# Kernel optimization log

Hardware: AMD Instinct MI355X
Metric: run time of the kernel (lower is better)

The kernel has to match this reference:

```python
import jax, jax.numpy as jnp
import numpy as np

K = 20                      # kNN size (init kwarg k)
_BN_S = 1.0 / np.sqrt(1.0 + 1e-5)  # BatchNorm eval with running var=1, mean=0


def _edge_conv(f, W1, b1, g, be, W2, b2):
    # f: [B,N,C]. DynamicEdgeConv: kNN in feature space (self included, as in
    # torch_cluster.knn), message = MLP([x_i, x_j - x_i]), max aggregation.
    sq = jnp.sum(f * f, -1)
    d = sq[:, :, None] + sq[:, None, :] - 2.0 * jnp.einsum('bnc,bmc->bnm', f, f)
    _, idx = jax.lax.top_k(-d, K)                      # [B,N,K]
    fj = jax.vmap(lambda fb, ib: fb[ib])(f, idx)       # [B,N,K,C] neighbor gather
    fi = jnp.broadcast_to(f[:, :, None, :], fj.shape)
    msg = jnp.concatenate([fi, fj - fi], -1)           # [B,N,K,2C]
    h = jax.nn.relu((msg @ W1 + b1) * (g * _BN_S) + be)  # Linear -> BN(eval) -> ReLU
    h = h @ W2 + b2                                    # plain last MLP layer
    return jnp.max(h, axis=2)                          # max over K neighbors


def _forward(x, pos,
             c1_W1, c1_b1, c1_g, c1_be, c1_W2, c1_b2,
             c2_W1, c2_b1, c2_g, c2_be, c2_W2, c2_b2,
             c3_W1, c3_b1, c3_g, c3_be, c3_W2, c3_b2,
             m_W1, m_b1, m_W2, m_b2, m_W3, m_b3, m_W4, m_b4):
    x0 = jnp.concatenate([x, pos], -1)                 # [B,N,6]
    x1 = _edge_conv(x0, c1_W1, c1_b1, c1_g, c1_be, c1_W2, c1_b2)
    x2 = _edge_conv(x1, c2_W1, c2_b1, c2_g, c2_be, c2_W2, c2_b2)
    x3 = _edge_conv(x2, c3_W1, c3_b1, c3_g, c3_be, c3_W2, c3_b2)
    h = jnp.concatenate([x1, x2, x3], -1)              # [B,N,192]
    # head MLP: norm=None, dropout inactive at inference, plain last layer
    h = jax.nn.relu(h @ m_W1 + m_b1)
    h = jax.nn.relu(h @ m_W2 + m_b2)
    h = jax.nn.relu(h @ m_W3 + m_b3)
    out = h @ m_W4 + m_b4                              # [B,N,40]
    return jax.nn.log_softmax(out, -1)


def setup_inputs() -> dict:
    key = jax.random.key(0)
    ks = iter(jax.random.split(key, 40))

    def lin(cin, cout):
        W = jax.random.normal(next(ks), (cin, cout), jnp.float32) / np.sqrt(cin)
        b = jnp.zeros((cout,), jnp.float32)
        return W, b

    inp = {}
    inp['x'] = jax.random.normal(next(ks), (8, 4096, 3), jnp.float32)
    inp['pos'] = jax.random.normal(next(ks), (8, 4096, 3), jnp.float32)
    for i, cin in zip((1, 2, 3), (12, 128, 128)):      # 2*in_channels of each conv
        W1, b1 = lin(cin, 64)
        W2, b2 = lin(64, 64)
        inp[f'c{i}_W1'], inp[f'c{i}_b1'] = W1, b1
        inp[f'c{i}_g'] = jnp.ones((64,), jnp.float32)
        inp[f'c{i}_be'] = jnp.zeros((64,), jnp.float32)
        inp[f'c{i}_W2'], inp[f'c{i}_b2'] = W2, b2
    dims = [192, 1024, 256, 128, 40]
    for j in range(4):
        W, b = lin(dims[j], dims[j + 1])
        inp[f'm_W{j + 1}'], inp[f'm_b{j + 1}'] = W, b
    return inp


def reference(x, pos,
              c1_W1, c1_b1, c1_g, c1_be, c1_W2, c1_b2,
              c2_W1, c2_b1, c2_g, c2_be, c2_W2, c2_b2,
              c3_W1, c3_b1, c3_g, c3_be, c3_W2, c3_b2,
              m_W1, m_b1, m_W2, m_b2, m_W3, m_b3, m_W4, m_b4):
    return _forward(x, pos,
                    c1_W1, c1_b1, c1_g, c1_be, c1_W2, c1_b2,
                    c2_W1, c2_b1, c2_g, c2_be, c2_W2, c2_b2,
                    c3_W1, c3_b1, c3_g, c3_be, c3_W2, c3_b2,
                    m_W1, m_b1, m_W2, m_b2, m_W3, m_b3, m_W4, m_b4)
```

## Files before the change

kernel.cpp:

```cpp
#include <hip/hip_runtime.h>
#include <math.h>

#define KNN 20
#define NPTS 4096
#define NB 8

__device__ __forceinline__ bool lexless(float d1, int i1, float d2, int i2) {
    return d1 < d2 || (d1 == d2 && i1 < i2);
}

__global__ __launch_bounds__(256) void concat_norm_kernel(const float* __restrict__ x,
                                                          const float* __restrict__ pos,
                                                          float* __restrict__ f0,
                                                          float* __restrict__ nrm, int total) {
    int p = blockIdx.x * 256 + threadIdx.x;
    if (p < total) {
        float v0 = x[(size_t)p*3 + 0], v1 = x[(size_t)p*3 + 1], v2 = x[(size_t)p*3 + 2];
        float v3 = pos[(size_t)p*3 + 0], v4 = pos[(size_t)p*3 + 1], v5 = pos[(size_t)p*3 + 2];
        f0[(size_t)p*6 + 0] = v0; f0[(size_t)p*6 + 1] = v1; f0[(size_t)p*6 + 2] = v2;
        f0[(size_t)p*6 + 3] = v3; f0[(size_t)p*6 + 4] = v4; f0[(size_t)p*6 + 5] = v5;
        float s = 0.f;
        s = fmaf(v0, v0, s); s = fmaf(v1, v1, s); s = fmaf(v2, v2, s);
        s = fmaf(v3, v3, s); s = fmaf(v4, v4, s); s = fmaf(v5, v5, s);
        nrm[p] = s;
    }
}

template<int C>
__global__ __launch_bounds__(256) void norm_kernel(const float* __restrict__ f, int ldf,
                                                   float* __restrict__ norms, int total) {
    int p = blockIdx.x * 256 + threadIdx.x;
    if (p >= total) return;
    const float* fp = f + (size_t)p * ldf;
    float s = 0.f;
    if constexpr ((C & 3) == 0) {
#pragma unroll
        for (int k = 0; k < C; k += 4) {
            float4 v = *(const float4*)(fp + k);
            s = fmaf(v.x, v.x, s); s = fmaf(v.y, v.y, s);
            s = fmaf(v.z, v.z, s); s = fmaf(v.w, v.w, s);
        }
    } else {
#pragma unroll
        for (int k = 0; k < C; ++k) s = fmaf(fp[k], fp[k], s);
    }
    norms[p] = s;
}

#define KCHAIN(ck_) do {                                                 \
    unsigned long long kc = (ck_);                                       \
    _Pragma("unroll")                                                    \
    for (int t = 0; t < KNN; ++t) {                                      \
        bool sw = kc < bk[t];                                            \
        unsigned long long nn = sw ? kc : bk[t];                         \
        unsigned long long oo = sw ? bk[t] : kc;                         \
        bk[t] = nn; kc = oo;                                             \
    }                                                                    \
} while (0)

#define PACKK(dv_, jv_, out_) do {                                       \
    unsigned pu = __float_as_uint(dv_);                                  \
    pu = (pu == 0x80000000u) ? 0u : pu;                    \
    pu ^= (unsigned)((int)pu >> 31) | 0x80000000u;                       \
    (out_) = ((unsigned long long)pu << 32) | (unsigned)(jv_);           \
} while (0)

#define PUSHF(dv_, jg_) do {                                             \
    if ((dv_) <= thr) {                                                  \
        pd5 = pd4; pj5 = pj4; pd4 = pd3; pj4 = pj3;                      \
        pd3 = pd2; pj3 = pj2; pd2 = pd1; pj2 = pj1;                      \
        pd1 = pd0; pj1 = pj0; pd0 = (dv_); pj0 = (jg_); ++cnt;           \
    }                                                                    \
} while (0)

#define FLUSHF() do {                                                    \
    if (cnt > 0) { unsigned long long k0_; PACKK(pd0, pj0, k0_); KCHAIN(k0_); } \
    if (cnt > 1) { unsigned long long k1_; PACKK(pd1, pj1, k1_); KCHAIN(k1_); } \
    if (cnt > 2) { unsigned long long k2_; PACKK(pd2, pj2, k2_); KCHAIN(k2_); } \
    if (cnt > 3) { unsigned long long k3_; PACKK(pd3, pj3, k3_); KCHAIN(k3_); } \
    if (cnt > 4) { unsigned long long k4_; PACKK(pd4, pj4, k4_); KCHAIN(k4_); } \
    if (cnt > 5) { unsigned long long k5_; PACKK(pd5, pj5, k5_); KCHAIN(k5_); } \
    cnt = 0;                                                             \
    unsigned hu_ = (unsigned)(bk[KNN - 1] >> 32);                        \
    atomicMin(&thrQ[q], hu_);                                            \
    hu_ = (hu_ & 0x80000000u) ? (hu_ ^ 0x80000000u) : ~hu_;              \
    thr = __uint_as_float(hu_);                                          \
} while (0)

#define KMERGE(ptr_) do {                                                \
    const unsigned long long* mp = (ptr_);                               \
    _Pragma("unroll 1")                                                  \
    for (int tm = 0; tm < KNN; ++tm) {                                   \
        unsigned long long mk = mp[tm];                                  \
        if (mk >= bk[KNN - 1]) break;                                    \
        KCHAIN(mk);                                                      \
    }                                                                    \
} while (0)

#define KSENTINEL 0xFF800000FFFFFFFFULL

template<int C>
__global__ __launch_bounds__(128, 2) void knn_tile_kernel(const float* __restrict__ f, int ldf,
                                                          const float* __restrict__ norms,
                                                          int* __restrict__ idx) {
    const int qb    = blockIdx.x * 32;
    const int b     = qb >> 12;
    const int qloc0 = qb & (NPTS - 1);
    const int tid   = threadIdx.x;
    const int q     = tid & 31;
    const int sub   = tid >> 5;
    const int tx    = tid & 15;
    const int ty    = tid >> 4;

    union __align__(16) SM {
        struct {
            float Qs[C][32];
            float Cs[C][64];
            float Ds[32][68];
        } a;
        unsigned long long md[32][2 * KNN + 1];
    };
    __shared__ SM sm;
    __shared__ unsigned thrQ[32];

    const float* fb = f + (size_t)b * NPTS * ldf;
    const float* nb = norms + (size_t)b * NPTS;

    if (tid < 32) thrQ[tid] = 0xFFFFFFFFu;

    if constexpr ((C & 15) == 0) {
        int m = tid >> 2, ko = (tid & 3) * 4;
        const float* src = fb + (size_t)(qloc0 + m) * ldf;
#pragma unroll
        for (int k4 = ko; k4 < C; k4 += 16) {
            float4 v = *(const float4*)(src + k4);
            sm.a.Qs[k4 + 0][m] = v.x; sm.a.Qs[k4 + 1][m] = v.y;
            sm.a.Qs[k4 + 2][m] = v.z; sm.a.Qs[k4 + 3][m] = v.w;
        }
    } else {
        for (int e = tid; e < C * 32; e += 128) {
            int k = e >> 5, m = e & 31;
            sm.a.Qs[k][m] = fb[(size_t)(qloc0 + m) * ldf + k];
        }
    }

    const float4 qnv = *(const float4*)(nb + qloc0 + ty * 4);
    const float qnr[4] = {qnv.x, qnv.y, qnv.z, qnv.w};

    unsigned long long bk[KNN];
#pragma unroll
    for (int t = 0; t < KNN; ++t) bk[t] = KSENTINEL;
    float thr = INFINITY;
    float pd0 = 0.f, pd1 = 0.f, pd2 = 0.f, pd3 = 0.f, pd4 = 0.f, pd5 = 0.f;
    int   pj0 = 0, pj1 = 0, pj2 = 0, pj3 = 0, pj4 = 0, pj5 = 0;
    int   cnt = 0;

    auto stageC = [&](int j0) {
        if constexpr ((C & 7) == 0) {
            int jj = tid >> 1, ko = (tid & 1) * 4;
            const float* src = fb + (size_t)(j0 + jj) * ldf;
#pragma unroll
            for (int k4 = ko; k4 < C; k4 += 8) {
                float4 v = *(const float4*)(src + k4);
                sm.a.Cs[k4 + 0][jj] = v.x; sm.a.Cs[k4 + 1][jj] = v.y;
                sm.a.Cs[k4 + 2][jj] = v.z; sm.a.Cs[k4 + 3][jj] = v.w;
            }
        } else {
            for (int e = tid; e < C * 64; e += 128) {
                int k = e >> 6, j = e & 63;
                sm.a.Cs[k][j] = fb[(size_t)(j0 + j) * ldf + k];
            }
        }
    };

    auto gemmT = [&](int j0) {
        float acc[4][4] = {};
#pragma unroll 8
        for (int kk = 0; kk < C; ++kk) {
            float4 av = *(const float4*)&sm.a.Qs[kk][ty * 4];
            float4 bv = *(const float4*)&sm.a.Cs[kk][tx * 4];
            float a[4] = {av.x, av.y, av.z, av.w};
            float bb[4] = {bv.x, bv.y, bv.z, bv.w};
#pragma unroll
            for (int i = 0; i < 4; ++i)
#pragma unroll
                for (int j = 0; j < 4; ++j) acc[i][j] = fmaf(a[i], bb[j], acc[i][j]);
        }
        const float4 cnv = *(const float4*)(nb + j0 + tx * 4);
#pragma unroll
        for (int i = 0; i < 4; ++i) {
            float4 o;
            o.x = fmaf(-2.0f, acc[i][0], qnr[i] + cnv.x);
            o.y = fmaf(-2.0f, acc[i][1], qnr[i] + cnv.y);
            o.z = fmaf(-2.0f, acc[i][2], qnr[i] + cnv.z);
            o.w = fmaf(-2.0f, acc[i][3], qnr[i] + cnv.w);
            *(float4*)&sm.a.Ds[ty * 4 + i][tx * 4] = o;
        }
    };

    auto scanT = [&](int j0) {
        {
            unsigned su = thrQ[q];
            unsigned hu = (su & 0x80000000u) ? (su ^ 0x80000000u) : ~su;
            thr = fminf(thr, __uint_as_float(hu));
        }
        const int jb = sub * 16;
        const float4 v0 = *(const float4*)&sm.a.Ds[q][jb + 0];
        const float4 v1 = *(const float4*)&sm.a.Ds[q][jb + 4];
        const float4 v2 = *(const float4*)&sm.a.Ds[q][jb + 8];
        const float4 v3 = *(const float4*)&sm.a.Ds[q][jb + 12];
        const int jg = j0 + jb;
        PUSHF(v0.x, jg + 0);  PUSHF(v0.y, jg + 1);
        PUSHF(v0.z, jg + 2);  PUSHF(v0.w, jg + 3);  if (__any(cnt >= 3)) FLUSHF();
        PUSHF(v1.x, jg + 4);  PUSHF(v1.y, jg + 5);
        PUSHF(v1.z, jg + 6);  PUSHF(v1.w, jg + 7);  if (__any(cnt >= 3)) FLUSHF();
        PUSHF(v2.x, jg + 8);  PUSHF(v2.y, jg + 9);
        PUSHF(v2.z, jg + 10); PUSHF(v2.w, jg + 11); if (__any(cnt >= 3)) FLUSHF();
        PUSHF(v3.x, jg + 12); PUSHF(v3.y, jg + 13);
        PUSHF(v3.z, jg + 14); PUSHF(v3.w, jg + 15);
        if (__any(cnt > 0)) FLUSHF();
    };

    stageC(0);
    __syncthreads();
    gemmT(0);
    __syncthreads();
#pragma unroll 1
    for (int t = 1; t < NPTS / 64; ++t) {
        stageC(t * 64);
        scanT((t - 1) * 64);
        __syncthreads();
        gemmT(t * 64);
        __syncthreads();
    }
    scanT(NPTS - 64);
    if (__any(cnt > 0)) FLUSHF();

    __syncthreads();
    if (sub >= 2) {
#pragma unroll
        for (int t = 0; t < KNN; ++t) sm.md[q][(sub - 2) * KNN + t] = bk[t];
    }
    __syncthreads();
    if (sub < 2) KMERGE(&sm.md[q][sub * KNN]);
    __syncthreads();
    if (sub == 1) {
#pragma unroll
        for (int t = 0; t < KNN; ++t) sm.md[q][t] = bk[t];
    }
    __syncthreads();
    if (sub == 0) {
        KMERGE(&sm.md[q][0]);
        int* op = idx + (size_t)(qb + q) * KNN;
#pragma unroll
        for (int t = 0; t < KNN; ++t) op[t] = (int)bk[t];
    }
}

__global__ __launch_bounds__(128, 2) void knn6_kernel(const float* __restrict__ f,
                                                      const float* __restrict__ norms,
                                                      int* __restrict__ idx) {
    const int qb    = blockIdx.x * 32;
    const int b     = qb >> 12;
    const int qloc0 = qb & (NPTS - 1);
    const int tid   = threadIdx.x;
    const int q     = tid & 31;
    const int sub   = tid >> 5;

    __shared__ __align__(16) float Cs[2][64][8];
    __shared__ unsigned long long md[32][2 * KNN + 1];
    __shared__ unsigned thrQ[32];

    const float* fb = f + (size_t)b * NPTS * 6;
    const float* nb = norms + (size_t)b * NPTS;

    if (tid < 32) thrQ[tid] = 0xFFFFFFFFu;

    float fir[6];
    {
        const float* qsrc = fb + (size_t)(qloc0 + q) * 6;
#pragma unroll
        for (int k = 0; k < 6; ++k) fir[k] = qsrc[k];
    }
    const float qn = nb[qloc0 + q];

    unsigned long long bk[KNN];
#pragma unroll
    for (int t = 0; t < KNN; ++t) bk[t] = KSENTINEL;
    float thr = INFINITY;
    float pd0 = 0.f, pd1 = 0.f, pd2 = 0.f, pd3 = 0.f, pd4 = 0.f, pd5 = 0.f;
    int   pj0 = 0, pj1 = 0, pj2 = 0, pj3 = 0, pj4 = 0, pj5 = 0;
    int   cnt = 0;

    auto stage6 = [&](int j0, int s) {
#pragma unroll
        for (int e = tid; e < 512; e += 128) {
            int j = e >> 3, k = e & 7;
            float v = 0.f;
            if (k < 6)       v = fb[(size_t)(j0 + j) * 6 + k];
            else if (k == 6) v = nb[j0 + j];
            Cs[s][j][k] = v;
        }
    };

    auto scan6 = [&](int j0, int s) {
        {
            unsigned su = thrQ[q];
            unsigned hu = (su & 0x80000000u) ? (su ^ 0x80000000u) : ~su;
            thr = fminf(thr, __uint_as_float(hu));
        }
        const int jb = sub * 16;
#pragma unroll
        for (int jj = 0; jj < 16; ++jj) {
            const float4 c0 = *(const float4*)&Cs[s][jb + jj][0];
            const float4 c1 = *(const float4*)&Cs[s][jb + jj][4];
            float dot = 0.f;
            dot = fmaf(fir[0], c0.x, dot);
            dot = fmaf(fir[1], c0.y, dot);
            dot = fmaf(fir[2], c0.z, dot);
            dot = fmaf(fir[3], c0.w, dot);
            dot = fmaf(fir[4], c1.x, dot);
            dot = fmaf(fir[5], c1.y, dot);
            float d = fmaf(-2.0f, dot, qn + c1.z);
            PUSHF(d, j0 + jb + jj);
            if ((jj & 3) == 3) { if (__any(cnt >= 3)) FLUSHF(); }
        }
        if (__any(cnt > 0)) FLUSHF();
    };

    stage6(0, 0);
    __syncthreads();
#pragma unroll 1
    for (int t = 0; t < NPTS / 64; ++t) {
        const int cur = t & 1;
        if (t + 1 < NPTS / 64) stage6((t + 1) * 64, cur ^ 1);
        scan6(t * 64, cur);
        __syncthreads();
    }
    if (__any(cnt > 0)) FLUSHF();

    if (sub >= 2) {
#pragma unroll
        for (int t = 0; t < KNN; ++t) md[q][(sub - 2) * KNN + t] = bk[t];
    }
    __syncthreads();
    if (sub < 2) KMERGE(&md[q][sub * KNN]);
    __syncthreads();
    if (sub == 1) {
#pragma unroll
        for (int t = 0; t < KNN; ++t) md[q][t] = bk[t];
    }
    __syncthreads();
    if (sub == 0) {
        KMERGE(&md[q][0]);
        int* op = idx + (size_t)(qb + q) * KNN;
#pragma unroll
        for (int t = 0; t < KNN; ++t) op[t] = (int)bk[t];
    }
}

template<int C>
__global__ __launch_bounds__(64) void edgeconv_kernel(
    const float* __restrict__ f, int ldf,
    const int* __restrict__ idx,
    const float* __restrict__ W1, const float* __restrict__ b1,
    const float* __restrict__ g,  const float* __restrict__ be,
    const float* __restrict__ W2, const float* __restrict__ b2,
    float* __restrict__ out, int ldo) {
    const int p = blockIdx.x;
    const int b = p >> 12;
    const int i = p & (NPTS - 1);
    const int c = threadIdx.x;
    __shared__ __align__(16) float fi_s[C];
    __shared__ __align__(16) float fj_s[KNN][C];
    __shared__ __align__(16) float h1_s[KNN][64];
    __shared__ int nidx[KNN];
    const float* fb = f + (size_t)b * NPTS * ldf;
    if (c < KNN) nidx[c] = idx[(size_t)p * KNN + c];
    if (c < C)   fi_s[c] = fb[(size_t)i * ldf + c];
    __syncthreads();
#pragma unroll
    for (int j = 0; j < KNN; ++j)
        if (c < C) fj_s[j][c] = fb[(size_t)nidx[j] * ldf + c];
    __syncthreads();
    float fir[C];
#pragma unroll
    for (int k = 0; k < C; ++k) fir[k] = fi_s[k];

    const float bn_s = (float)(1.0 / sqrt(1.0 + 1e-5));
    const float bnscale = g[c] * bn_s;
    float base = b1[c];
#pragma unroll
    for (int k = 0; k < C; ++k) base = fmaf(fir[k], W1[k * 64 + c], base);
    float acc[KNN];
#pragma unroll
    for (int j = 0; j < KNN; ++j) acc[j] = base;

    if constexpr ((C & 3) == 0) {
#pragma unroll
        for (int k = 0; k < C; k += 4) {
            float w0 = W1[(C + k + 0) * 64 + c];
            float w1 = W1[(C + k + 1) * 64 + c];
            float w2 = W1[(C + k + 2) * 64 + c];
            float w3 = W1[(C + k + 3) * 64 + c];
            float f0 = fir[k + 0], f1 = fir[k + 1], f2 = fir[k + 2], f3 = fir[k + 3];
#pragma unroll
            for (int j = 0; j < KNN; ++j) {
                float4 v = *(const float4*)&fj_s[j][k];
                acc[j] = fmaf(v.x - f0, w0, acc[j]);
                acc[j] = fmaf(v.y - f1, w1, acc[j]);
                acc[j] = fmaf(v.z - f2, w2, acc[j]);
                acc[j] = fmaf(v.w - f3, w3, acc[j]);
            }
        }
    } else {
#pragma unroll
        for (int k = 0; k < C; ++k) {
            float w = W1[(C + k) * 64 + c];
            float fik = fir[k];
#pragma unroll
            for (int j = 0; j < KNN; ++j) acc[j] = fmaf(fj_s[j][k] - fik, w, acc[j]);
        }
    }
    float bec = be[c];
#pragma unroll
    for (int j = 0; j < KNN; ++j) h1_s[j][c] = fmaxf(fmaf(acc[j], bnscale, bec), 0.f);
    __syncthreads();

    float acc2[KNN];
    float b2c = b2[c];
#pragma unroll
    for (int j = 0; j < KNN; ++j) acc2[j] = b2c;
#pragma unroll
    for (int k = 0; k < 64; k += 4) {
        float w0 = W2[(k + 0) * 64 + c];
        float w1 = W2[(k + 1) * 64 + c];
        float w2 = W2[(k + 2) * 64 + c];
        float w3 = W2[(k + 3) * 64 + c];
#pragma unroll
        for (int j = 0; j < KNN; ++j) {
            float4 v = *(const float4*)&h1_s[j][k];
            acc2[j] = fmaf(v.x, w0, acc2[j]);
            acc2[j] = fmaf(v.y, w1, acc2[j]);
            acc2[j] = fmaf(v.z, w2, acc2[j]);
            acc2[j] = fmaf(v.w, w3, acc2[j]);
        }
    }
    float m = acc2[0];
#pragma unroll
    for (int j = 1; j < KNN; ++j) m = fmaxf(m, acc2[j]);
    out[(size_t)p * ldo + c] = m;
}

__global__ __launch_bounds__(256) void repack_w1_kernel(const float* __restrict__ W1,
                                                        const float* __restrict__ b1,
                                                        float* __restrict__ Wp,
                                                        float* __restrict__ bp) {
    int t = blockIdx.x * 256 + threadIdx.x;
    if (t < 64 * 64) {
        int k = t >> 6, c = t & 63;
        Wp[k * 128 + c]      = W1[k * 64 + c];
        Wp[k * 128 + 64 + c] = W1[(64 + k) * 64 + c];
    }
    if (t < 128) bp[t] = (t < 64) ? b1[t] : 0.f;
}

__global__ __launch_bounds__(64) void edgeconv_fact_kernel(
    const float* __restrict__ GH,
    const int* __restrict__ idx,
    const float* __restrict__ g,  const float* __restrict__ be,
    const float* __restrict__ W2, const float* __restrict__ b2,
    float* __restrict__ out, int ldo) {
    const int p = blockIdx.x;
    const int b = p >> 12;
    const int c = threadIdx.x;
    __shared__ __align__(16) float h1_s[KNN][64];
    __shared__ int nidx[KNN];
    if (c < KNN) nidx[c] = idx[(size_t)p * KNN + c];
    const float H = GH[(size_t)p * 128 + c];
    const float G = GH[(size_t)p * 128 + 64 + c];
    const float hb = H - G;
    const float bn_s = (float)(1.0 / sqrt(1.0 + 1e-5));
    const float bnscale = g[c] * bn_s;
    const float bec = be[c];
    const float* GHb = GH + (size_t)b * NPTS * 128 + 64;
    __syncthreads();
#pragma unroll
    for (int j = 0; j < KNN; ++j) {
        float gj = GHb[(size_t)nidx[j] * 128 + c];
        h1_s[j][c] = fmaxf(fmaf(hb + gj, bnscale, bec), 0.f);
    }
    __syncthreads();

    float acc2[KNN];
    float b2c = b2[c];
#pragma unroll
    for (int j = 0; j < KNN; ++j) acc2[j] = b2c;
#pragma unroll
    for (int k = 0; k < 64; k += 4) {
        float w0 = W2[(k + 0) * 64 + c];
        float w1 = W2[(k + 1) * 64 + c];
        float w2 = W2[(k + 2) * 64 + c];
        float w3 = W2[(k + 3) * 64 + c];
#pragma unroll
        for (int j = 0; j < KNN; ++j) {
            float4 v = *(const float4*)&h1_s[j][k];
            acc2[j] = fmaf(v.x, w0, acc2[j]);
            acc2[j] = fmaf(v.y, w1, acc2[j]);
            acc2[j] = fmaf(v.z, w2, acc2[j]);
            acc2[j] = fmaf(v.w, w3, acc2[j]);
        }
    }
    float m = acc2[0];
#pragma unroll
    for (int j = 1; j < KNN; ++j) m = fmaxf(m, acc2[j]);
    out[(size_t)p * ldo + c] = m;
}

template<bool RELU>
__global__ __launch_bounds__(256, 2) void gemm_kernel(
    const float* __restrict__ A, int lda,
    const float* __restrict__ W,
    const float* __restrict__ bias,
    float* __restrict__ Cc, int ldc,
    int N, int K) {
    const int BM = 128, BN = 128, BK = 16;
    __shared__ __align__(16) float As[16][128 + 4];
    __shared__ __align__(16) float Bs[16][128 + 4];
    const int bm = blockIdx.y * BM;
    const int bn = blockIdx.x * BN;
    const int tid = threadIdx.x;
    const int tx = tid & 15, ty = tid >> 4;
    float acc[8][8] = {};
    for (int k0 = 0; k0 < K; k0 += BK) {
        {
            int r = tid >> 2;
            int kq = (tid & 3) * 4;
#pragma unroll
            for (int h = 0; h < 2; ++h) {
                int rr = r + h * 64;
                float4 v = *(const float4*)(A + (size_t)(bm + rr) * lda + k0 + kq);
                As[kq + 0][rr] = v.x; As[kq + 1][rr] = v.y;
                As[kq + 2][rr] = v.z; As[kq + 3][rr] = v.w;
            }
        }
        {
            int kk = tid >> 4;
            int n8 = (tid & 15) * 8;
            float4 v0 = *(const float4*)(W + (size_t)(k0 + kk) * N + bn + n8);
            float4 v1 = *(const float4*)(W + (size_t)(k0 + kk) * N + bn + n8 + 4);
            *(float4*)&Bs[kk][n8] = v0;
            *(float4*)&Bs[kk][n8 + 4] = v1;
        }
        __syncthreads();
#pragma unroll
        for (int kk = 0; kk < BK; ++kk) {
            float4 a0 = *(const float4*)&As[kk][ty * 8];
            float4 a1 = *(const float4*)&As[kk][ty * 8 + 4];
            float4 b0 = *(const float4*)&Bs[kk][tx * 8];
            float4 b1 = *(const float4*)&Bs[kk][tx * 8 + 4];
            float a[8] = {a0.x, a0.y, a0.z, a0.w, a1.x, a1.y, a1.z, a1.w};
            float bb[8] = {b0.x, b0.y, b0.z, b0.w, b1.x, b1.y, b1.z, b1.w};
#pragma unroll
            for (int i = 0; i < 8; ++i)
#pragma unroll
                for (int j = 0; j < 8; ++j) acc[i][j] = fmaf(a[i], bb[j], acc[i][j]);
        }
        __syncthreads();
    }
    const float4 bi0 = *(const float4*)(bias + bn + tx * 8);
    const float4 bi1 = *(const float4*)(bias + bn + tx * 8 + 4);
    const float bb[8] = {bi0.x, bi0.y, bi0.z, bi0.w, bi1.x, bi1.y, bi1.z, bi1.w};
#pragma unroll
    for (int i = 0; i < 8; ++i) {
        int m = bm + ty * 8 + i;
        float4 o0, o1;
        o0.x = acc[i][0] + bb[0]; o0.y = acc[i][1] + bb[1];
        o0.z = acc[i][2] + bb[2]; o0.w = acc[i][3] + bb[3];
        o1.x = acc[i][4] + bb[4]; o1.y = acc[i][5] + bb[5];
        o1.z = acc[i][6] + bb[6]; o1.w = acc[i][7] + bb[7];
        if (RELU) {
            o0.x = fmaxf(o0.x, 0.f); o0.y = fmaxf(o0.y, 0.f);
            o0.z = fmaxf(o0.z, 0.f); o0.w = fmaxf(o0.w, 0.f);
            o1.x = fmaxf(o1.x, 0.f); o1.y = fmaxf(o1.y, 0.f);
            o1.z = fmaxf(o1.z, 0.f); o1.w = fmaxf(o1.w, 0.f);
        }
        *(float4*)(Cc + (size_t)m * ldc + bn + tx * 8) = o0;
        *(float4*)(Cc + (size_t)m * ldc + bn + tx * 8 + 4) = o1;
    }
}

__global__ __launch_bounds__(64) void head_kernel(const float* __restrict__ h3,
                                                  const float* __restrict__ W4,
                                                  const float* __restrict__ b4,
                                                  float* __restrict__ out) {
    const int p = blockIdx.x;
    const int lane = threadIdx.x;
    const float* hp = h3 + (size_t)p * 128;
    float v = -INFINITY;
    if (lane < 40) {
        float acc = b4[lane];
#pragma unroll
        for (int k = 0; k < 128; ++k) acc = fmaf(hp[k], W4[k * 40 + lane], acc);
        v = acc;
    }
    float mx = v;
#pragma unroll
    for (int s = 1; s < 64; s <<= 1) mx = fmaxf(mx, __shfl_xor(mx, s));
    float e = (lane < 40) ? expf(v - mx) : 0.0f;
    float se = e;
#pragma unroll
    for (int s = 1; s < 64; s <<= 1) se += __shfl_xor(se, s);
    if (lane < 40) out[(size_t)p * 40 + lane] = v - mx - logf(se);
}

extern "C" void kernel_launch(void* const* d_in, const int* in_sizes, int n_in,
                              void* d_out, int out_size, void* d_ws, size_t ws_size,
                              hipStream_t stream) {
    (void)in_sizes; (void)n_in; (void)out_size;
    const float* x     = (const float*)d_in[0];
    const float* pos   = (const float*)d_in[1];
    const float* c1_W1 = (const float*)d_in[2];
    const float* c1_b1 = (const float*)d_in[3];
    const float* c1_g  = (const float*)d_in[4];
    const float* c1_be = (const float*)d_in[5];
    const float* c1_W2 = (const float*)d_in[6];
    const float* c1_b2 = (const float*)d_in[7];
    const float* c2_W1 = (const float*)d_in[8];
    const float* c2_b1 = (const float*)d_in[9];
    const float* c2_g  = (const float*)d_in[10];
    const float* c2_be = (const float*)d_in[11];
    const float* c2_W2 = (const float*)d_in[12];
    const float* c2_b2 = (const float*)d_in[13];
    const float* c3_W1 = (const float*)d_in[14];
    const float* c3_b1 = (const float*)d_in[15];
    const float* c3_g  = (const float*)d_in[16];
    const float* c3_be = (const float*)d_in[17];
    const float* c3_W2 = (const float*)d_in[18];
    const float* c3_b2 = (const float*)d_in[19];
    const float* m_W1  = (const float*)d_in[20];
    const float* m_b1  = (const float*)d_in[21];
    const float* m_W2  = (const float*)d_in[22];
    const float* m_b2  = (const float*)d_in[23];
    const float* m_W3  = (const float*)d_in[24];
    const float* m_b3  = (const float*)d_in[25];
    const float* m_W4  = (const float*)d_in[26];
    const float* m_b4  = (const float*)d_in[27];
    float* out = (float*)d_out;

    const int TOT = NB * NPTS;

    float* ws   = (float*)d_ws;
    float* f0   = ws;
    int*   idxb = (int*)(ws + 196608);
    float* feat = ws + 196608 + 655360;

    const size_t basef  = 196608 + 655360 + 6291456;
    const size_t availf = ws_size / 4;
    int MC = 4096;
    if (availf >= basef + (size_t)32768 * 1408) MC = 32768;
    else if (availf >= basef + (size_t)16384 * 1408) MC = 16384;
    else if (availf >= basef + (size_t)8192 * 1408) MC = 8192;

    float* h1   = feat + 6291456;
    float* h2   = h1 + (size_t)MC * 1024;
    float* h3   = h2 + (size_t)MC * 256;
    float* nrm  = h1;
    float* GH   = h1 + 131072;
    float* Wp   = GH + (size_t)TOT * 128;
    float* bp   = Wp + 8192;

    concat_norm_kernel<<<(TOT + 255) / 256, 256, 0, stream>>>(x, pos, f0, nrm, TOT);
    knn6_kernel<<<TOT / 32, 128, 0, stream>>>(f0, nrm, idxb);
    edgeconv_kernel<6><<<TOT, 64, 0, stream>>>(f0, 6, idxb,
        c1_W1, c1_b1, c1_g, c1_be, c1_W2, c1_b2, feat + 0, 192);

    norm_kernel<64><<<(TOT + 255) / 256, 256, 0, stream>>>(feat + 0, 192, nrm, TOT);
    knn_tile_kernel<64><<<TOT / 32, 128, 0, stream>>>(feat + 0, 192, nrm, idxb);
    repack_w1_kernel<<<16, 256, 0, stream>>>(c2_W1, c2_b1, Wp, bp);
    gemm_kernel<false><<<dim3(1, TOT / 128), 256, 0, stream>>>(
        feat + 0, 192, Wp, bp, GH, 128, 128, 64);
    edgeconv_fact_kernel<<<TOT, 64, 0, stream>>>(GH, idxb,
        c2_g, c2_be, c2_W2, c2_b2, feat + 64, 192);

    norm_kernel<64><<<(TOT + 255) / 256, 256, 0, stream>>>(feat + 64, 192, nrm, TOT);
    knn_tile_kernel<64><<<TOT / 32, 128, 0, stream>>>(feat + 64, 192, nrm, idxb);
    repack_w1_kernel<<<16, 256, 0, stream>>>(c3_W1, c3_b1, Wp, bp);
    gemm_kernel<false><<<dim3(1, TOT / 128), 256, 0, stream>>>(
        feat + 64, 192, Wp, bp, GH, 128, 128, 64);
    edgeconv_fact_kernel<<<TOT, 64, 0, stream>>>(GH, idxb,
        c3_g, c3_be, c3_W2, c3_b2, feat + 128, 192);

    for (int mc = 0; mc < TOT; mc += MC) {
        gemm_kernel<true><<<dim3(1024 / 128, MC / 128), 256, 0, stream>>>(
            feat + (size_t)mc * 192, 192, m_W1, m_b1, h1, 1024, 1024, 192);
        gemm_kernel<true><<<dim3(256 / 128, MC / 128), 256, 0, stream>>>(
            h1, 1024, m_W2, m_b2, h2, 256, 256, 1024);
        gemm_kernel<true><<<dim3(128 / 128, MC / 128), 256, 0, stream>>>(
            h2, 256, m_W3, m_b3, h3, 128, 128, 256);
        head_kernel<<<MC, 64, 0, stream>>>(h3, m_W4, m_b4, out + (size_t)mc * 40);
    }
}
```

Baseline: 2.146 ms.

## Factorize first EdgeConv, register-cache query features in kNN, batch head kernel

Layer 1 now uses the same factorized path as layers 2 and 3. A small per-point kernel computes the x_i and x_j terms of W1 once, and the existing edgeconv_fact_kernel reuses them instead of redoing the 6-channel MLP for every edge. The kNN tile GEMM keeps the first 32 query channels in registers rather than reading them from shared memory each step, which raises register pressure. The head kernel processes four points per 256-thread block and stages W4 in shared memory to cut repeated global loads.

```diff
diff --git a/kernel.cpp b/kernel.cpp
--- a/kernel.cpp
+++ b/kernel.cpp
@@ -147,6 +147,20 @@
     const float4 qnv = *(const float4*)(nb + qloc0 + ty * 4);
     const float qnr[4] = {qnv.x, qnv.y, qnv.z, qnv.w};
 
+    float qa[4][32];
+    if constexpr (C >= 32 && (C & 3) == 0) {
+#pragma unroll
+        for (int i = 0; i < 4; ++i) {
+            const float* src = fb + (size_t)(qloc0 + ty * 4 + i) * ldf;
+#pragma unroll
+            for (int kq = 0; kq < 8; ++kq) {
+                float4 v = *(const float4*)(src + kq * 4);
+                qa[i][kq * 4 + 0] = v.x; qa[i][kq * 4 + 1] = v.y;
+                qa[i][kq * 4 + 2] = v.z; qa[i][kq * 4 + 3] = v.w;
+            }
+        }
+    }
+
     unsigned long long bk[KNN];
 #pragma unroll
     for (int t = 0; t < KNN; ++t) bk[t] = KSENTINEL;
@@ -175,16 +189,39 @@
 
     auto gemmT = [&](int j0) {
         float acc[4][4] = {};
+        if constexpr (C >= 32 && (C & 3) == 0) {
+#pragma unroll
+            for (int kk = 0; kk < 32; ++kk) {
+                float4 bv = *(const float4*)&sm.a.Cs[kk][tx * 4];
+                float bb[4] = {bv.x, bv.y, bv.z, bv.w};
+#pragma unroll
+                for (int i = 0; i < 4; ++i)
+#pragma unroll
+                    for (int j = 0; j < 4; ++j) acc[i][j] = fmaf(qa[i][kk], bb[j], acc[i][j]);
+            }
 #pragma unroll 8
-        for (int kk = 0; kk < C; ++kk) {
-            float4 av = *(const float4*)&sm.a.Qs[kk][ty * 4];
-            float4 bv = *(const float4*)&sm.a.Cs[kk][tx * 4];
-            float a[4] = {av.x, av.y, av.z, av.w};
-            float bb[4] = {bv.x, bv.y, bv.z, bv.w};
-#pragma unroll
-            for (int i = 0; i < 4; ++i)
-#pragma unroll
-                for (int j = 0; j < 4; ++j) acc[i][j] = fmaf(a[i], bb[j], acc[i][j]);
+            for (int kk = 32; kk < C; ++kk) {
+                float4 av = *(const float4*)&sm.a.Qs[kk][ty * 4];
+                float4 bv = *(const float4*)&sm.a.Cs[kk][tx * 4];
+                float a[4] = {av.x, av.y, av.z, av.w};
+                float bb[4] = {bv.x, bv.y, bv.z, bv.w};
+#pragma unroll
+                for (int i = 0; i < 4; ++i)
+#pragma unroll
+                    for (int j = 0; j < 4; ++j) acc[i][j] = fmaf(a[i], bb[j], acc[i][j]);
+            }
+        } else {
+#pragma unroll 8
+            for (int kk = 0; kk < C; ++kk) {
+                float4 av = *(const float4*)&sm.a.Qs[kk][ty * 4];
+                float4 bv = *(const float4*)&sm.a.Cs[kk][tx * 4];
+                float a[4] = {av.x, av.y, av.z, av.w};
+                float bb[4] = {bv.x, bv.y, bv.z, bv.w};
+#pragma unroll
+                for (int i = 0; i < 4; ++i)
+#pragma unroll
+                    for (int j = 0; j < 4; ++j) acc[i][j] = fmaf(a[i], bb[j], acc[i][j]);
+            }
         }
         const float4 cnv = *(const float4*)(nb + j0 + tx * 4);
 #pragma unroll
@@ -359,97 +396,22 @@
     }
 }
 
-template<int C>
-__global__ __launch_bounds__(64) void edgeconv_kernel(
-    const float* __restrict__ f, int ldf,
-    const int* __restrict__ idx,
-    const float* __restrict__ W1, const float* __restrict__ b1,
-    const float* __restrict__ g,  const float* __restrict__ be,
-    const float* __restrict__ W2, const float* __restrict__ b2,
-    float* __restrict__ out, int ldo) {
-    const int p = blockIdx.x;
-    const int b = p >> 12;
-    const int i = p & (NPTS - 1);
-    const int c = threadIdx.x;
-    __shared__ __align__(16) float fi_s[C];
-    __shared__ __align__(16) float fj_s[KNN][C];
-    __shared__ __align__(16) float h1_s[KNN][64];
-    __shared__ int nidx[KNN];
-    const float* fb = f + (size_t)b * NPTS * ldf;
-    if (c < KNN) nidx[c] = idx[(size_t)p * KNN + c];
-    if (c < C)   fi_s[c] = fb[(size_t)i * ldf + c];
-    __syncthreads();
-#pragma unroll
-    for (int j = 0; j < KNN; ++j)
-        if (c < C) fj_s[j][c] = fb[(size_t)nidx[j] * ldf + c];
-    __syncthreads();
-    float fir[C];
-#pragma unroll
-    for (int k = 0; k < C; ++k) fir[k] = fi_s[k];
-
-    const float bn_s = (float)(1.0 / sqrt(1.0 + 1e-5));
-    const float bnscale = g[c] * bn_s;
-    float base = b1[c];
-#pragma unroll
-    for (int k = 0; k < C; ++k) base = fmaf(fir[k], W1[k * 64 + c], base);
-    float acc[KNN];
-#pragma unroll
-    for (int j = 0; j < KNN; ++j) acc[j] = base;
-
-    if constexpr ((C & 3) == 0) {
-#pragma unroll
-        for (int k = 0; k < C; k += 4) {
-            float w0 = W1[(C + k + 0) * 64 + c];
-            float w1 = W1[(C + k + 1) * 64 + c];
-            float w2 = W1[(C + k + 2) * 64 + c];
-            float w3 = W1[(C + k + 3) * 64 + c];
-            float f0 = fir[k + 0], f1 = fir[k + 1], f2 = fir[k + 2], f3 = fir[k + 3];
-#pragma unroll
-            for (int j = 0; j < KNN; ++j) {
-                float4 v = *(const float4*)&fj_s[j][k];
-                acc[j] = fmaf(v.x - f0, w0, acc[j]);
-                acc[j] = fmaf(v.y - f1, w1, acc[j]);
-                acc[j] = fmaf(v.z - f2, w2, acc[j]);
-                acc[j] = fmaf(v.w - f3, w3, acc[j]);
-            }
-        }
-    } else {
-#pragma unroll
-        for (int k = 0; k < C; ++k) {
-            float w = W1[(C + k) * 64 + c];
-            float fik = fir[k];
-#pragma unroll
-            for (int j = 0; j < KNN; ++j) acc[j] = fmaf(fj_s[j][k] - fik, w, acc[j]);
-        }
-    }
-    float bec = be[c];
-#pragma unroll
-    for (int j = 0; j < KNN; ++j) h1_s[j][c] = fmaxf(fmaf(acc[j], bnscale, bec), 0.f);
-    __syncthreads();
-
-    float acc2[KNN];
-    float b2c = b2[c];
-#pragma unroll
-    for (int j = 0; j < KNN; ++j) acc2[j] = b2c;
-#pragma unroll
-    for (int k = 0; k < 64; k += 4) {
-        float w0 = W2[(k + 0) * 64 + c];
-        float w1 = W2[(k + 1) * 64 + c];
-        float w2 = W2[(k + 2) * 64 + c];
-        float w3 = W2[(k + 3) * 64 + c];
-#pragma unroll
-        for (int j = 0; j < KNN; ++j) {
-            float4 v = *(const float4*)&h1_s[j][k];
-            acc2[j] = fmaf(v.x, w0, acc2[j]);
-            acc2[j] = fmaf(v.y, w1, acc2[j]);
-            acc2[j] = fmaf(v.z, w2, acc2[j]);
-            acc2[j] = fmaf(v.w, w3, acc2[j]);
-        }
-    }
-    float m = acc2[0];
-#pragma unroll
-    for (int j = 1; j < KNN; ++j) m = fmaxf(m, acc2[j]);
-    out[(size_t)p * ldo + c] = m;
+__global__ __launch_bounds__(256) void hg6_kernel(const float* __restrict__ f0,
+                                                  const float* __restrict__ W1,
+                                                  const float* __restrict__ b1,
+                                                  float* __restrict__ GH, int total) {
+    int t = blockIdx.x * 256 + threadIdx.x;
+    if (t >= total * 128) return;
+    int p  = t >> 7;
+    int cc = t & 127;
+    int c  = cc & 63;
+    bool isG = cc >= 64;
+    const float* fp = f0 + (size_t)p * 6;
+    const float* Wb = W1 + (isG ? 6 * 64 : 0);
+    float acc = isG ? 0.f : b1[c];
+#pragma unroll
+    for (int k = 0; k < 6; ++k) acc = fmaf(fp[k], Wb[k * 64 + c], acc);
+    GH[(size_t)p * 128 + cc] = acc;
 }
 
 __global__ __launch_bounds__(256) void repack_w1_kernel(const float* __restrict__ W1,
@@ -590,18 +552,25 @@
     }
 }
 
-__global__ __launch_bounds__(64) void head_kernel(const float* __restrict__ h3,
-                                                  const float* __restrict__ W4,
-                                                  const float* __restrict__ b4,
-                                                  float* __restrict__ out) {
-    const int p = blockIdx.x;
-    const int lane = threadIdx.x;
-    const float* hp = h3 + (size_t)p * 128;
+__global__ __launch_bounds__(256) void head_kernel(const float* __restrict__ h3,
+                                                   const float* __restrict__ W4,
+                                                   const float* __restrict__ b4,
+                                                   float* __restrict__ out) {
+    __shared__ float W4s[128 * 40];
+    __shared__ float hps[4][128];
+    const int tid  = threadIdx.x;
+    const int w    = tid >> 6;
+    const int lane = tid & 63;
+    const int p    = blockIdx.x * 4 + w;
+    for (int e = tid; e < 128 * 40; e += 256) W4s[e] = W4[e];
+    if (lane < 32)
+        *(float4*)&hps[w][lane * 4] = *(const float4*)(h3 + (size_t)p * 128 + lane * 4);
+    __syncthreads();
     float v = -INFINITY;
     if (lane < 40) {
         float acc = b4[lane];
 #pragma unroll
-        for (int k = 0; k < 128; ++k) acc = fmaf(hp[k], W4[k * 40 + lane], acc);
+        for (int k = 0; k < 128; ++k) acc = fmaf(hps[w][k], W4s[k * 40 + lane], acc);
         v = acc;
     }
     float mx = v;
@@ -672,8 +641,9 @@
 
     concat_norm_kernel<<<(TOT + 255) / 256, 256, 0, stream>>>(x, pos, f0, nrm, TOT);
     knn6_kernel<<<TOT / 32, 128, 0, stream>>>(f0, nrm, idxb);
-    edgeconv_kernel<6><<<TOT, 64, 0, stream>>>(f0, 6, idxb,
-        c1_W1, c1_b1, c1_g, c1_be, c1_W2, c1_b2, feat + 0, 192);
+    hg6_kernel<<<(TOT * 128) / 256, 256, 0, stream>>>(f0, c1_W1, c1_b1, GH, TOT);
+    edgeconv_fact_kernel<<<TOT, 64, 0, stream>>>(GH, idxb,
+        c1_g, c1_be, c1_W2, c1_b2, feat + 0, 192);
 
     norm_kernel<64><<<(TOT + 255) / 256, 256, 0, stream>>>(feat + 0, 192, nrm, TOT);
     knn_tile_kernel<64><<<TOT / 32, 128, 0, stream>>>(feat + 0, 192, nrm, idxb);
@@ -698,6 +668,6 @@
             h1, 1024, m_W2, m_b2, h2, 256, 256, 1024);
         gemm_kernel<true><<<dim3(128 / 128, MC / 128), 256, 0, stream>>>(
             h2, 256, m_W3, m_b3, h3, 128, 128, 256);
-        head_kernel<<<MC, 64, 0, stream>>>(h3, m_W4, m_b4, out + (size_t)mc * 40);
-    }
-}
+        head_kernel<<<MC / 4, 256, 0, stream>>>(h3, m_W4, m_b4, out + (size_t)mc * 40);
+    }
+}
```

New measurement: 3.314 ms. +54.4%, slower.
